# Kernel optimization log

Measured on AMD Instinct MI355X. Metric: run time of the kernel, lower is better.

The kernel has to match this reference:

```python
import jax, jax.numpy as jnp
import numpy as np

NUMSTEPS = 10  # message-passing rounds (SeqGGNN numsteps)

def setup_inputs() -> dict:
    key = jax.random.key(0)
    ks = jax.random.split(key, 10)
    B, S, H, V = 64, 512, 256, 32000
    s = 0.05  # keep activations in a stable range
    return {
        "x": jax.random.randint(ks[0], (B, S), 0, V),
        "emb": jax.random.normal(ks[1], (V, H), jnp.float32) * s,
        "W_edge": jax.random.normal(ks[2], (3, H, H), jnp.float32) * s,  # [fwd, bwd, self]
        "b_edge": jax.random.normal(ks[3], (3, H), jnp.float32) * s,
        "W_ih": jax.random.normal(ks[4], (3 * H, H), jnp.float32) * s,
        "W_hh": jax.random.normal(ks[5], (3 * H, H), jnp.float32) * s,
        "b_ih": jax.random.normal(ks[6], (3 * H,), jnp.float32) * s,
        "b_hh": jax.random.normal(ks[7], (3 * H,), jnp.float32) * s,
        "out_w": jax.random.normal(ks[8], (V, H), jnp.float32) * s,
        "out_b": jax.random.normal(ks[9], (V,), jnp.float32) * s,
    }

def _gru(m, h, W_ih, W_hh, b_ih, b_hh):
    # torch.nn.GRUCell semantics with input m, state h
    gi = m @ W_ih.T + b_ih
    gh = h @ W_hh.T + b_hh
    i_r, i_z, i_n = jnp.split(gi, 3, axis=-1)
    h_r, h_z, h_n = jnp.split(gh, 3, axis=-1)
    r = jax.nn.sigmoid(i_r + h_r)
    z = jax.nn.sigmoid(i_z + h_z)
    n = jnp.tanh(i_n + r * h_n)
    return (1.0 - z) * n + z * h

def reference(x, emb, W_edge, b_edge, W_ih, W_hh, b_ih, b_hh, out_w, out_b):
    # x: [B,S] int ids; chain graph per row with 3 edge types:
    #   fwd:  j -> j+1 (node j+1 receives W_edge[0] h_j + b_edge[0])
    #   bwd:  j+1 -> j (node j receives W_edge[1] h_{j+1} + b_edge[1])
    #   self: j -> j   (W_edge[2] h_j + b_edge[2])
    h0 = emb[x]  # [B,S,H]

    def step(h, _):
        t_fwd = jnp.einsum('bsh,hk->bsk', h, W_edge[0]) + b_edge[0]
        t_bwd = jnp.einsum('bsh,hk->bsk', h, W_edge[1]) + b_edge[1]
        m_self = jnp.einsum('bsh,hk->bsk', h, W_edge[2]) + b_edge[2]
        # scatter-sum along the chain == shift with zero pad at boundaries
        m_fwd = jnp.pad(t_fwd[:, :-1], ((0, 0), (1, 0), (0, 0)))
        m_bwd = jnp.pad(t_bwd[:, 1:], ((0, 0), (0, 1), (0, 0)))
        m = m_fwd + m_bwd + m_self
        h_new = _gru(m, h, W_ih, W_hh, b_ih, b_hh)
        return h_new, None

    h, _ = jax.lax.scan(step, h0, None, length=NUMSTEPS)
    last = h[:, -1, :]  # [B,H]
    return last @ out_w.T + out_b  # [B,V]
```

## Files before the change

### kernel.cpp

```cpp
#include <hip/hip_runtime.h>
#include <math.h>

#define Bb 64
#define Ss 512
#define Hh 256
#define Vv 32000
#define BS (Bb*Ss)
#define NSTEPS 10

typedef __attribute__((ext_vector_type(8))) short bf16x8;
typedef __attribute__((ext_vector_type(4))) float f32x4;
typedef unsigned short u16;

#define MFMA(a,b,c) __builtin_amdgcn_mfma_f32_16x16x32_bf16((a),(b),(c),0,0,0)

__device__ __forceinline__ u16 f2bf(float f) {
    unsigned u = __float_as_uint(f);
    u += 0x7fffu + ((u >> 16) & 1u);
    return (u16)(u >> 16);
}
__device__ __forceinline__ float bf2f(u16 h) {
    return __uint_as_float(((unsigned)h) << 16);
}
__device__ __forceinline__ int nmap(int j, int g) {
    return ((j >> 4) << 6) | (g << 4) | (j & 15);
}
#define GLL(src, dst) __builtin_amdgcn_global_load_lds( \
    (const __attribute__((address_space(1))) void*)(src), \
    (__attribute__((address_space(3))) void*)(dst), 16, 0, 0)

__global__ __launch_bounds__(256)
void k_prep_big(const float* __restrict__ We, const float* __restrict__ Wih,
                const float* __restrict__ Whh, u16* __restrict__ Bbig) {
    __shared__ u16 Aps[64 * 32];
    __shared__ u16 Bps[64 * 32];
    const int p = blockIdx.y, seg = p / 3, g = p % 3;
    const int segmap0 = (seg == 0) ? 2 : (seg == 1 ? 0 : 1);
    const float* Wseg = We + segmap0 * 65536;
    const int kt = (blockIdx.x >> 2) * 64, jt = (blockIdx.x & 3) * 64;
    const int t = threadIdx.x;
    const int lane = t & 63, wid = t >> 6;
    const int wy = (wid >> 1) * 32, wx = (wid & 1) * 32;
    const int lr = lane & 15, hi = lane >> 4;

    f32x4 acc[2][2];
    #pragma unroll
    for (int a = 0; a < 2; ++a)
        #pragma unroll
        for (int b = 0; b < 2; ++b) acc[a][b] = 0.0f;

    for (int ks = 0; ks < 8; ++ks) {
        const int k0 = ks * 32;
        {
            int r = t >> 2, kc = t & 3;
            const float* sa = Wseg + (kt + r) * 256 + k0 + kc * 8;
            float4 a0 = *(const float4*)sa, a1 = *(const float4*)(sa + 4);
            bf16x8 va;
            va[0]=(short)f2bf(a0.x); va[1]=(short)f2bf(a0.y); va[2]=(short)f2bf(a0.z); va[3]=(short)f2bf(a0.w);
            va[4]=(short)f2bf(a1.x); va[5]=(short)f2bf(a1.y); va[6]=(short)f2bf(a1.z); va[7]=(short)f2bf(a1.w);
            ((bf16x8*)Aps)[r * 4 + (kc ^ (r & 3))] = va;
            const float* sb = Wih + (g * 256 + jt + r) * 256 + k0 + kc * 8;
            float4 b0 = *(const float4*)sb, b1 = *(const float4*)(sb + 4);
            bf16x8 vb;
            vb[0]=(short)f2bf(b0.x); vb[1]=(short)f2bf(b0.y); vb[2]=(short)f2bf(b0.z); vb[3]=(short)f2bf(b0.w);
            vb[4]=(short)f2bf(b1.x); vb[5]=(short)f2bf(b1.y); vb[6]=(short)f2bf(b1.z); vb[7]=(short)f2bf(b1.w);
            ((bf16x8*)Bps)[r * 4 + (kc ^ (r & 3))] = vb;
        }
        __syncthreads();
        bf16x8 af[2], bfv[2];
        #pragma unroll
        for (int f = 0; f < 2; ++f) {
            int ra = wy + f * 16 + lr;
            af[f]  = ((const bf16x8*)Aps)[ra * 4 + (hi ^ (ra & 3))];
            int rb = wx + f * 16 + lr;
            bfv[f] = ((const bf16x8*)Bps)[rb * 4 + (hi ^ (rb & 3))];
        }
        #pragma unroll
        for (int fm = 0; fm < 2; ++fm)
            #pragma unroll
            for (int fn = 0; fn < 2; ++fn)
                acc[fm][fn] = MFMA(af[fm], bfv[fn], acc[fm][fn]);
        __syncthreads();
    }
    #pragma unroll
    for (int fm = 0; fm < 2; ++fm)
        #pragma unroll
        for (int fn = 0; fn < 2; ++fn) {
            int kbase = kt + wy + fm * 16 + hi * 4;
            int j     = jt + wx + fn * 16 + lr;
            float4 wv = make_float4(0.f, 0.f, 0.f, 0.f);
            if (seg == 0 && g < 2)
                wv = *(const float4*)(Whh + (g * 256 + j) * 256 + kbase);
            ushort4 o;
            o.x = f2bf(acc[fm][fn][0] + wv.x);
            o.y = f2bf(acc[fm][fn][1] + wv.y);
            o.z = f2bf(acc[fm][fn][2] + wv.z);
            o.w = f2bf(acc[fm][fn][3] + wv.w);
            *(ushort4*)(Bbig + (size_t)nmap(j, g) * 768 + seg * 256 + kbase) = o;
        }
}

__global__ __launch_bounds__(256)
void k_prep_hn(const float* __restrict__ Whh, u16* __restrict__ Bbig) {
    int j = blockIdx.x / 3;
    int k = (blockIdx.x % 3) * 256 + threadIdx.x;
    Bbig[(size_t)nmap(j, 3) * 768 + k] =
        (k < 256) ? f2bf(Whh[(512 + j) * 256 + k]) : (u16)0;
}

__global__ __launch_bounds__(256)
void k_prep_bias(const float* __restrict__ Wih, const float* __restrict__ b_edge,
                 const float* __restrict__ b_ih, const float* __restrict__ b_hh,
                 float* __restrict__ bias) {
    int id = blockIdx.x * 256 + threadIdx.x;
    int c = id >> 10, n = id & 1023;
    int g = (n >> 4) & 3;
    int j = ((n >> 6) << 4) | (n & 15);
    float a;
    if (g == 3) {
        a = b_hh[512 + j];
    } else {
        a = b_ih[g * 256 + j] + (g < 2 ? b_hh[g * 256 + j] : 0.f);
        const float* wrow = Wih + (g * 256 + j) * 256;
        for (int k = 0; k < 256; ++k) {
            float eb = b_edge[512 + k] + (c != 0 ? b_edge[k] : 0.f)
                     + (c != 2 ? b_edge[256 + k] : 0.f);
            a += eb * wrow[k];
        }
    }
    bias[c * 1024 + n] = a;
}

__global__ __launch_bounds__(256)
void k_prep_zp(u16* __restrict__ zp) {
    zp[blockIdx.x * 256 + threadIdx.x] = 0;
}

__global__ __launch_bounds__(256)
void k_embed(const int* __restrict__ x, const float* __restrict__ emb,
             u16* __restrict__ h) {
    int idx = blockIdx.x * 256 + threadIdx.x;
    int row = idx >> 5, c8 = idx & 31;
    long long tok = x[row];
    const float4* e = reinterpret_cast<const float4*>(emb + tok * Hh + c8 * 8);
    float4 a = e[0], b = e[1];
    bf16x8 v;
    v[0]=(short)f2bf(a.x); v[1]=(short)f2bf(a.y); v[2]=(short)f2bf(a.z); v[3]=(short)f2bf(a.w);
    v[4]=(short)f2bf(b.x); v[5]=(short)f2bf(b.y); v[6]=(short)f2bf(b.z); v[7]=(short)f2bf(b.w);
    ((bf16x8*)h)[idx] = v;
}

__global__ __launch_bounds__(512)
void k_step(const u16* __restrict__ hin, const u16* __restrict__ Bbig,
            const float* __restrict__ bias, const u16* __restrict__ zp,
            u16* __restrict__ hout) {
    __shared__ u16 As[128 * 64];
    __shared__ u16 Bs[256 * 64];
    const int t = threadIdx.x;
    const int lane = t & 63, wid = t >> 6;
    const int rowBlk = blockIdx.y * 128;
    const int colBlk = blockIdx.x * 256;
    const int wy = wid >> 2, wx = wid & 3;
    const int lr = lane & 15, hi = lane >> 4;
    const int s0 = rowBlk & (Ss - 1);

    const u16* srcB[4];
    u16* dstB[4];
    #pragma unroll
    for (int j = 0; j < 4; ++j) {
        int c = wid * 256 + j * 64 + lane;
        int r = c >> 3, kc = c & 7;
        srcB[j] = Bbig + (size_t)(colBlk + r) * 768 + (kc ^ (r & 7)) * 8;
        dstB[j] = Bs + wid * 2048 + j * 512;
    }
    u16* dstA[2];
    int  rA[2], kcA[2];
    #pragma unroll
    for (int j = 0; j < 2; ++j) {
        int c = wid * 128 + j * 64 + lane;
        rA[j] = c >> 3; kcA[j] = c & 7;
        dstA[j] = As + wid * 1024 + j * 512;
    }

    f32x4 acc[4][4];
    #pragma unroll
    for (int a = 0; a < 4; ++a)
        #pragma unroll
        for (int b = 0; b < 4; ++b) acc[a][b] = 0.0f;

    #pragma unroll 1
    for (int seg = 0; seg < 3; ++seg) {
        const int d = (seg == 0) ? 0 : (seg == 1 ? -1 : 1);
        const u16* srcA[2];
        #pragma unroll
        for (int j = 0; j < 2; ++j) {
            int ss = s0 + rA[j] + d;
            srcA[j] = (ss >= 0 && ss < Ss)
                ? hin + (size_t)(rowBlk + rA[j] + d) * Hh + (kcA[j] ^ (rA[j] & 7)) * 8
                : zp;
        }
        #pragma unroll 1
        for (int k4 = 0; k4 < 4; ++k4) {
            GLL(srcA[0], dstA[0]);  srcA[0] += 64;
            GLL(srcA[1], dstA[1]);  srcA[1] += 64;
            #pragma unroll
            for (int j = 0; j < 4; ++j) { GLL(srcB[j], dstB[j]); srcB[j] += 64; }
            __syncthreads();
            #pragma unroll
            for (int kk = 0; kk < 2; ++kk) {
                bf16x8 af[4], bfv[4];
                #pragma unroll
                for (int f = 0; f < 4; ++f) {
                    int ra = wy * 64 + f * 16 + lr;
                    af[f] = ((const bf16x8*)As)[ra * 8 + ((kk * 4 + hi) ^ (ra & 7))];
                    int rb = wx * 64 + f * 16 + lr;
                    bfv[f] = ((const bf16x8*)Bs)[rb * 8 + ((kk * 4 + hi) ^ (rb & 7))];
                }
                #pragma unroll
                for (int fm = 0; fm < 4; ++fm)
                    #pragma unroll
                    for (int fn = 0; fn < 4; ++fn)
                        acc[fm][fn] = MFMA(af[fm], bfv[fn], acc[fm][fn]);
            }
            __syncthreads();
        }
    }
    const int hcol  = (blockIdx.x * 4 + wx) * 16 + lr;
    const int nbase = colBlk + wx * 64 + lr;
    #pragma unroll
    for (int fm = 0; fm < 4; ++fm)
        #pragma unroll
        for (int i = 0; i < 4; ++i) {
            int row = rowBlk + wy * 64 + fm * 16 + hi * 4 + i;
            int s = row & (Ss - 1);
            int cls = (s == 0) ? 0 : ((s == Ss - 1) ? 2 : 1);
            const float* bp = bias + cls * 1024 + nbase;
            float vr = acc[fm][0][i] + bp[0];
            float vz = acc[fm][1][i] + bp[16];
            float vn = acc[fm][2][i] + bp[32];
            float vh = acc[fm][3][i] + bp[48];
            float r = 1.f / (1.f + __expf(-vr));
            float z = 1.f / (1.f + __expf(-vz));
            float e = __expf(2.f * (vn + r * vh));
            float n = 1.f - 2.f / (e + 1.f);
            float hold = bf2f(hin[(size_t)row * Hh + hcol]);
            hout[(size_t)row * Hh + hcol] = f2bf(n + z * (hold - n));
        }
}

__global__ __launch_bounds__(256)
void k_out(const u16* __restrict__ h, const float* __restrict__ out_w,
           const float* __restrict__ out_b, float* __restrict__ out) {
    __shared__ u16 As[64 * 256];
    const int t = threadIdx.x;
    const int lane = t & 63, wid = t >> 6;
    const int colBlk = blockIdx.x * 128;
    const int wc = wid * 32;
    const int lr = lane & 15, hi = lane >> 4;

    #pragma unroll
    for (int i = 0; i < 8; ++i) {
        int c = t + i * 256;
        int r = c >> 5, kc = c & 31;
        bf16x8 v = *(const bf16x8*)(h + ((size_t)(r * Ss + (Ss - 1))) * Hh + kc * 8);
        ((bf16x8*)As)[r * 32 + (kc ^ (r & 7))] = v;
    }
    __syncthreads();

    f32x4 acc[4][2];
    #pragma unroll
    for (int a = 0; a < 4; ++a) { acc[a][0] = 0.0f; acc[a][1] = 0.0f; }

    #pragma unroll
    for (int ks = 0; ks < 8; ++ks) {
        bf16x8 af[4];
        #pragma unroll
        for (int f = 0; f < 4; ++f) {
            int ra = f * 16 + lr;
            af[f] = ((const bf16x8*)As)[ra * 32 + ((ks * 4 + hi) ^ (ra & 7))];
        }
        #pragma unroll
        for (int fn = 0; fn < 2; ++fn) {
            int n = colBlk + wc + fn * 16 + lr;
            const float* wp = out_w + (size_t)n * 256 + ks * 32 + hi * 8;
            float4 w0 = *(const float4*)wp, w1 = *(const float4*)(wp + 4);
            bf16x8 vb;
            vb[0]=(short)f2bf(w0.x); vb[1]=(short)f2bf(w0.y); vb[2]=(short)f2bf(w0.z); vb[3]=(short)f2bf(w0.w);
            vb[4]=(short)f2bf(w1.x); vb[5]=(short)f2bf(w1.y); vb[6]=(short)f2bf(w1.z); vb[7]=(short)f2bf(w1.w);
            #pragma unroll
            for (int fm = 0; fm < 4; ++fm)
                acc[fm][fn] = MFMA(af[fm], vb, acc[fm][fn]);
        }
    }
    #pragma unroll
    for (int fm = 0; fm < 4; ++fm)
        #pragma unroll
        for (int fn = 0; fn < 2; ++fn)
            #pragma unroll
            for (int i = 0; i < 4; ++i) {
                int row = fm * 16 + hi * 4 + i;
                int col = colBlk + wc + fn * 16 + lr;
                out[(size_t)row * Vv + col] = acc[fm][fn][i] + out_b[col];
            }
}

extern "C" void kernel_launch(void* const* d_in, const int* in_sizes, int n_in,
                              void* d_out, int out_size, void* d_ws, size_t ws_size,
                              hipStream_t stream) {
    const int*   x      = (const int*)  d_in[0];
    const float* emb    = (const float*)d_in[1];
    const float* W_edge = (const float*)d_in[2];
    const float* b_edge = (const float*)d_in[3];
    const float* W_ih   = (const float*)d_in[4];
    const float* W_hh   = (const float*)d_in[5];
    const float* b_ih   = (const float*)d_in[6];
    const float* b_hh   = (const float*)d_in[7];
    const float* out_w  = (const float*)d_in[8];
    const float* out_b  = (const float*)d_in[9];
    float* out = (float*)d_out;

    u16* hA   = (u16*)d_ws;
    u16* hB   = hA + (size_t)BS * Hh;
    u16* Bbig = hB + (size_t)BS * Hh;
    float* bias = (float*)(Bbig + (size_t)1024 * 768);
    u16* zp   = (u16*)(bias + 3 * 1024);

    k_prep_big <<<dim3(16, 9), 256, 0, stream>>>(W_edge, W_ih, W_hh, Bbig);
    k_prep_hn  <<<768, 256, 0, stream>>>(W_hh, Bbig);
    k_prep_bias<<<12, 256, 0, stream>>>(W_ih, b_edge, b_ih, b_hh, bias);
    k_prep_zp  <<<2, 256, 0, stream>>>(zp);
    k_embed    <<<BS * Hh / 8 / 256, 256, 0, stream>>>(x, emb, hA);

    u16* cur = hA;
    u16* nxt = hB;
    for (int step = 0; step < NSTEPS; ++step) {
        k_step<<<dim3(4, BS / 128), 512, 0, stream>>>(cur, Bbig, bias, zp, nxt);
        u16* tmp = cur; cur = nxt; nxt = tmp;
    }
    k_out<<<Vv / 128, 256, 0, stream>>>(cur, out_w, out_b, out);
}
```

Measured before the change: 642.3 us.

## Stage full A tile with halo rows once, double-buffer B, skip zero MFMAs

The step kernel now loads the whole 128-row h tile plus two halo rows into shared memory once and reuses it for the three shifted segments, instead of reloading shifted A slices per segment. B tiles are double-buffered with explicit vmcnt waits and raw barriers, so the next load overlaps the current MFMAs. MFMAs for the fourth column group in the shifted segments are skipped because those weight blocks are zero. Shared memory grows to roughly 130 KB, which limits occupancy to one block per CU and makes correctness depend on manual waitcnt handling.

```diff
diff --git a/kernel.cpp b/kernel.cpp
--- a/kernel.cpp
+++ b/kernel.cpp
@@ -154,8 +154,8 @@
 void k_step(const u16* __restrict__ hin, const u16* __restrict__ Bbig,
             const float* __restrict__ bias, const u16* __restrict__ zp,
             u16* __restrict__ hout) {
-    __shared__ u16 As[128 * 64];
-    __shared__ u16 Bs[256 * 64];
+    __shared__ __attribute__((aligned(16))) u16 As[130 * 256];
+    __shared__ __attribute__((aligned(16))) u16 Bs[2][256 * 64];
     const int t = threadIdx.x;
     const int lane = t & 63, wid = t >> 6;
     const int rowBlk = blockIdx.y * 128;
@@ -164,22 +164,43 @@
     const int lr = lane & 15, hi = lane >> 4;
     const int s0 = rowBlk & (Ss - 1);
 
+    #pragma unroll
+    for (int i = 0; i < 8; ++i) {
+        int c = wid * 512 + i * 64 + lane;
+        int r = c >> 5, ci = c & 31;
+        GLL(hin + (size_t)(rowBlk + r) * Hh + ((ci ^ (r & 7)) << 3),
+            As + (size_t)(wid * 512 + i * 64) * 8);
+    }
+    if (wid == 0) {
+        int ci = lane & 31;
+        const u16* src;
+        if (lane < 32)
+            src = (s0 > 0)   ? hin + (size_t)(rowBlk - 1) * Hh + (ci << 3)
+                             : zp + (ci << 3);
+        else
+            src = (s0 < 384) ? hin + (size_t)(rowBlk + 128) * Hh + ((ci ^ 1) << 3)
+                             : zp + (ci << 3);
+        GLL(src, As + 128 * 256);
+    }
     const u16* srcB[4];
-    u16* dstB[4];
     #pragma unroll
     for (int j = 0; j < 4; ++j) {
         int c = wid * 256 + j * 64 + lane;
         int r = c >> 3, kc = c & 7;
-        srcB[j] = Bbig + (size_t)(colBlk + r) * 768 + (kc ^ (r & 7)) * 8;
-        dstB[j] = Bs + wid * 2048 + j * 512;
-    }
-    u16* dstA[2];
-    int  rA[2], kcA[2];
-    #pragma unroll
-    for (int j = 0; j < 2; ++j) {
-        int c = wid * 128 + j * 64 + lane;
-        rA[j] = c >> 3; kcA[j] = c & 7;
-        dstA[j] = As + wid * 1024 + j * 512;
+        srcB[j] = Bbig + (size_t)(colBlk + r) * 768 + ((kc ^ (r & 7)) << 3);
+    }
+    #pragma unroll
+    for (int j = 0; j < 4; ++j) {
+        GLL(srcB[j], Bs[0] + (wid * 256 + j * 64) * 8);
+        srcB[j] += 64;
+    }
+    int rowA0[4], rowA1[4], rowA2[4];
+    #pragma unroll
+    for (int f = 0; f < 4; ++f) {
+        int ra = wy * 64 + f * 16 + lr;
+        rowA0[f] = ra;
+        rowA1[f] = (ra == 0)   ? 128 : ra - 1;
+        rowA2[f] = (ra == 127) ? 129 : ra + 1;
     }
 
     f32x4 acc[4][4];
@@ -188,42 +209,45 @@
         #pragma unroll
         for (int b = 0; b < 4; ++b) acc[a][b] = 0.0f;
 
-    #pragma unroll 1
-    for (int seg = 0; seg < 3; ++seg) {
-        const int d = (seg == 0) ? 0 : (seg == 1 ? -1 : 1);
-        const u16* srcA[2];
-        #pragma unroll
-        for (int j = 0; j < 2; ++j) {
-            int ss = s0 + rA[j] + d;
-            srcA[j] = (ss >= 0 && ss < Ss)
-                ? hin + (size_t)(rowBlk + rA[j] + d) * Hh + (kcA[j] ^ (rA[j] & 7)) * 8
-                : zp;
-        }
-        #pragma unroll 1
-        for (int k4 = 0; k4 < 4; ++k4) {
-            GLL(srcA[0], dstA[0]);  srcA[0] += 64;
-            GLL(srcA[1], dstA[1]);  srcA[1] += 64;
-            #pragma unroll
-            for (int j = 0; j < 4; ++j) { GLL(srcB[j], dstB[j]); srcB[j] += 64; }
-            __syncthreads();
-            #pragma unroll
-            for (int kk = 0; kk < 2; ++kk) {
-                bf16x8 af[4], bfv[4];
+    #pragma unroll
+    for (int seg = 0; seg < 3; ++seg)
+    #pragma unroll
+    for (int k4 = 0; k4 < 4; ++k4) {
+        const int it = seg * 4 + k4;
+        const int buf = it & 1;
+        if (it < 11) {
+            #pragma unroll
+            for (int j = 0; j < 4; ++j) {
+                GLL(srcB[j], Bs[buf ^ 1] + (wid * 256 + j * 64) * 8);
+                srcB[j] += 64;
+            }
+            asm volatile("s_waitcnt vmcnt(4)" ::: "memory");
+        } else {
+            asm volatile("s_waitcnt vmcnt(0)" ::: "memory");
+        }
+        __builtin_amdgcn_s_barrier();
+        __builtin_amdgcn_sched_barrier(0);
+        #pragma unroll
+        for (int kk = 0; kk < 2; ++kk) {
+            bf16x8 af[4], bfv[4];
+            #pragma unroll
+            for (int f = 0; f < 4; ++f) {
+                int rr = (seg == 0) ? rowA0[f] : (seg == 1) ? rowA1[f] : rowA2[f];
+                af[f] = ((const bf16x8*)As)[rr * 32 + ((k4 * 8 + kk * 4 + hi) ^ (rr & 7))];
+            }
+            #pragma unroll
+            for (int f = 0; f < 4; ++f) {
+                int rb = wx * 64 + f * 16 + lr;
+                bfv[f] = ((const bf16x8*)Bs[buf])[rb * 8 + ((kk * 4 + hi) ^ (rb & 7))];
+            }
+            #pragma unroll
+            for (int fm = 0; fm < 4; ++fm)
                 #pragma unroll
-                for (int f = 0; f < 4; ++f) {
-                    int ra = wy * 64 + f * 16 + lr;
-                    af[f] = ((const bf16x8*)As)[ra * 8 + ((kk * 4 + hi) ^ (ra & 7))];
-                    int rb = wx * 64 + f * 16 + lr;
-                    bfv[f] = ((const bf16x8*)Bs)[rb * 8 + ((kk * 4 + hi) ^ (rb & 7))];
-                }
-                #pragma unroll
-                for (int fm = 0; fm < 4; ++fm)
-                    #pragma unroll
-                    for (int fn = 0; fn < 4; ++fn)
+                for (int fn = 0; fn < 4; ++fn)
+                    if (seg == 0 || fn < 3)
                         acc[fm][fn] = MFMA(af[fm], bfv[fn], acc[fm][fn]);
-            }
-            __syncthreads();
-        }
+        }
+        __builtin_amdgcn_s_barrier();
     }
     const int hcol  = (blockIdx.x * 4 + wx) * 16 + lr;
     const int nbase = colBlk + wx * 64 + lr;
```

New measurement: 654.7 us. About the same (+1.9%).

## Use 4-wave blocks with 64x128 warp tiles and skip zero hn blocks

Applied to the files above, without the earlier changes.

The step GEMM kernel moves from 8 waves to 4 waves per block, so each wave now computes a 64x128 output tile (4x8 MFMA fragments) and reuses each A fragment across twice as many B fragments. For the shifted-neighbour segments it also skips the fourth fragment of each gate group (the hn columns, which only take the unshifted h input), which removes about a quarter of the MFMAs and B LDS reads in two of the three segments. The larger per-wave tile doubles accumulator registers and halves waves per block, which can lower occupancy and latency hiding.

```diff
diff --git a/kernel.cpp b/kernel.cpp
--- a/kernel.cpp
+++ b/kernel.cpp
@@ -150,102 +150,113 @@
     ((bf16x8*)h)[idx] = v;
 }
 
-__global__ __launch_bounds__(512)
+__global__ __launch_bounds__(256)
 void k_step(const u16* __restrict__ hin, const u16* __restrict__ Bbig,
             const float* __restrict__ bias, const u16* __restrict__ zp,
             u16* __restrict__ hout) {
-    __shared__ u16 As[128 * 64];
-    __shared__ u16 Bs[256 * 64];
+    __shared__ __attribute__((aligned(16))) u16 As[128 * 64];
+    __shared__ __attribute__((aligned(16))) u16 Bs[256 * 64];
     const int t = threadIdx.x;
     const int lane = t & 63, wid = t >> 6;
     const int rowBlk = blockIdx.y * 128;
     const int colBlk = blockIdx.x * 256;
-    const int wy = wid >> 2, wx = wid & 3;
+    const int wy = wid >> 1, wx = wid & 1;
     const int lr = lane & 15, hi = lane >> 4;
     const int s0 = rowBlk & (Ss - 1);
 
-    const u16* srcB[4];
-    u16* dstB[4];
+    const u16* srcB[8];
+    u16* dstB[8];
+    #pragma unroll
+    for (int j = 0; j < 8; ++j) {
+        int c = t + j * 256;
+        int r = c >> 3, kc = c & 7;
+        srcB[j] = Bbig + (size_t)(colBlk + r) * 768 + ((kc ^ (r & 7)) << 3);
+        dstB[j] = Bs + (size_t)(j * 256 + wid * 64) * 8;
+    }
+    u16* dstA[4];
+    int  rA[4], kcA[4];
     #pragma unroll
     for (int j = 0; j < 4; ++j) {
-        int c = wid * 256 + j * 64 + lane;
-        int r = c >> 3, kc = c & 7;
-        srcB[j] = Bbig + (size_t)(colBlk + r) * 768 + (kc ^ (r & 7)) * 8;
-        dstB[j] = Bs + wid * 2048 + j * 512;
-    }
-    u16* dstA[2];
-    int  rA[2], kcA[2];
-    #pragma unroll
-    for (int j = 0; j < 2; ++j) {
-        int c = wid * 128 + j * 64 + lane;
+        int c = t + j * 256;
         rA[j] = c >> 3; kcA[j] = c & 7;
-        dstA[j] = As + wid * 1024 + j * 512;
-    }
-
-    f32x4 acc[4][4];
+        dstA[j] = As + (size_t)(j * 256 + wid * 64) * 8;
+    }
+
+    f32x4 acc[4][8];
     #pragma unroll
     for (int a = 0; a < 4; ++a)
         #pragma unroll
-        for (int b = 0; b < 4; ++b) acc[a][b] = 0.0f;
+        for (int b = 0; b < 8; ++b) acc[a][b] = 0.0f;
 
     #pragma unroll 1
     for (int seg = 0; seg < 3; ++seg) {
         const int d = (seg == 0) ? 0 : (seg == 1 ? -1 : 1);
-        const u16* srcA[2];
-        #pragma unroll
-        for (int j = 0; j < 2; ++j) {
+        const u16* srcA[4];
+        #pragma unroll
+        for (int j = 0; j < 4; ++j) {
             int ss = s0 + rA[j] + d;
             srcA[j] = (ss >= 0 && ss < Ss)
-                ? hin + (size_t)(rowBlk + rA[j] + d) * Hh + (kcA[j] ^ (rA[j] & 7)) * 8
+                ? hin + (size_t)(rowBlk + rA[j] + d) * Hh + ((kcA[j] ^ (rA[j] & 7)) << 3)
                 : zp;
         }
         #pragma unroll 1
         for (int k4 = 0; k4 < 4; ++k4) {
-            GLL(srcA[0], dstA[0]);  srcA[0] += 64;
-            GLL(srcA[1], dstA[1]);  srcA[1] += 64;
-            #pragma unroll
-            for (int j = 0; j < 4; ++j) { GLL(srcB[j], dstB[j]); srcB[j] += 64; }
+            #pragma unroll
+            for (int j = 0; j < 4; ++j) { GLL(srcA[j], dstA[j]); srcA[j] += 64; }
+            #pragma unroll
+            for (int j = 0; j < 8; ++j) { GLL(srcB[j], dstB[j]); srcB[j] += 64; }
             __syncthreads();
             #pragma unroll
             for (int kk = 0; kk < 2; ++kk) {
-                bf16x8 af[4], bfv[4];
+                bf16x8 af[4];
                 #pragma unroll
                 for (int f = 0; f < 4; ++f) {
                     int ra = wy * 64 + f * 16 + lr;
                     af[f] = ((const bf16x8*)As)[ra * 8 + ((kk * 4 + hi) ^ (ra & 7))];
-                    int rb = wx * 64 + f * 16 + lr;
-                    bfv[f] = ((const bf16x8*)Bs)[rb * 8 + ((kk * 4 + hi) ^ (rb & 7))];
                 }
                 #pragma unroll
-                for (int fm = 0; fm < 4; ++fm)
+                for (int fq = 0; fq < 2; ++fq) {
+                    bf16x8 bfv[4];
                     #pragma unroll
-                    for (int fn = 0; fn < 4; ++fn)
-                        acc[fm][fn] = MFMA(af[fm], bfv[fn], acc[fm][fn]);
+                    for (int f = 0; f < 4; ++f) {
+                        if (seg != 0 && f == 3) continue;
+                        int rb = wx * 128 + (fq * 4 + f) * 16 + lr;
+                        bfv[f] = ((const bf16x8*)Bs)[rb * 8 + ((kk * 4 + hi) ^ (rb & 7))];
+                    }
+                    #pragma unroll
+                    for (int fm = 0; fm < 4; ++fm)
+                        #pragma unroll
+                        for (int f = 0; f < 4; ++f)
+                            if (seg == 0 || f < 3)
+                                acc[fm][fq * 4 + f] = MFMA(af[fm], bfv[f], acc[fm][fq * 4 + f]);
+                }
             }
             __syncthreads();
         }
     }
-    const int hcol  = (blockIdx.x * 4 + wx) * 16 + lr;
-    const int nbase = colBlk + wx * 64 + lr;
+    const int hq = (colBlk >> 2) + wx * 32;
     #pragma unroll
     for (int fm = 0; fm < 4; ++fm)
         #pragma unroll
-        for (int i = 0; i < 4; ++i) {
-            int row = rowBlk + wy * 64 + fm * 16 + hi * 4 + i;
-            int s = row & (Ss - 1);
-            int cls = (s == 0) ? 0 : ((s == Ss - 1) ? 2 : 1);
-            const float* bp = bias + cls * 1024 + nbase;
-            float vr = acc[fm][0][i] + bp[0];
-            float vz = acc[fm][1][i] + bp[16];
-            float vn = acc[fm][2][i] + bp[32];
-            float vh = acc[fm][3][i] + bp[48];
-            float r = 1.f / (1.f + __expf(-vr));
-            float z = 1.f / (1.f + __expf(-vz));
-            float e = __expf(2.f * (vn + r * vh));
-            float n = 1.f - 2.f / (e + 1.f);
-            float hold = bf2f(hin[(size_t)row * Hh + hcol]);
-            hout[(size_t)row * Hh + hcol] = f2bf(n + z * (hold - n));
-        }
+        for (int fq = 0; fq < 2; ++fq)
+            #pragma unroll
+            for (int i = 0; i < 4; ++i) {
+                int row = rowBlk + wy * 64 + fm * 16 + hi * 4 + i;
+                int s = row & (Ss - 1);
+                int cls = (s == 0) ? 0 : ((s == Ss - 1) ? 2 : 1);
+                const float* bp = bias + cls * 1024 + colBlk + wx * 128 + fq * 64 + lr;
+                float vr = acc[fm][fq * 4 + 0][i] + bp[0];
+                float vz = acc[fm][fq * 4 + 1][i] + bp[16];
+                float vn = acc[fm][fq * 4 + 2][i] + bp[32];
+                float vh = acc[fm][fq * 4 + 3][i] + bp[48];
+                float r = 1.f / (1.f + __expf(-vr));
+                float z = 1.f / (1.f + __expf(-vz));
+                float e = __expf(2.f * (vn + r * vh));
+                float n = 1.f - 2.f / (e + 1.f);
+                int hcol = hq + fq * 16 + lr;
+                float hold = bf2f(hin[(size_t)row * Hh + hcol]);
+                hout[(size_t)row * Hh + hcol] = f2bf(n + z * (hold - n));
+            }
 }
 
 __global__ __launch_bounds__(256)
@@ -334,7 +345,7 @@
     u16* cur = hA;
     u16* nxt = hB;
     for (int step = 0; step < NSTEPS; ++step) {
-        k_step<<<dim3(4, BS / 128), 512, 0, stream>>>(cur, Bbig, bias, zp, nxt);
+        k_step<<<dim3(4, BS / 128), 256, 0, stream>>>(cur, Bbig, bias, zp, nxt);
         u16* tmp = cur; cur = nxt; nxt = tmp;
     }
     k_out<<<Vv / 128, 256, 0, stream>>>(cur, out_w, out_b, out);
```

New measurement: 977.6 us. 1.52x slower.
